# Performance work log

Measured on AMD Instinct MI355X. Metric: run time of the kernel, lower is better.

The kernel has to match this reference:

```python
import jax, jax.numpy as jnp
import numpy as np

D_HALF = 255
H = 2 * D_HALF + 1   # 511 channels (2*d+1)
L = 2048             # sequence length
N = 32               # S4D complex state modes per channel
NLAYERS = 4          # l
EPS = 1e-5


def setup_inputs() -> dict:
    key = jax.random.key(0)
    ks = jax.random.split(key, 10)
    Z = jax.random.normal(ks[0], (H, L), dtype=jnp.float32)
    # S4D-Lin initialization
    dt_min, dt_max = 1e-3, 1e-1
    log_dt = (jax.random.uniform(ks[1], (H,), dtype=jnp.float32)
              * (np.log(dt_max) - np.log(dt_min)) + np.log(dt_min))
    A_real_log = jnp.log(0.5 * jnp.ones((H, N), dtype=jnp.float32))
    A_imag = jnp.pi * jnp.broadcast_to(jnp.arange(N, dtype=jnp.float32), (H, N))
    C_re = jax.random.normal(ks[2], (H, N), dtype=jnp.float32)
    C_im = jax.random.normal(ks[3], (H, N), dtype=jnp.float32)
    D_skip = jax.random.normal(ks[4], (H,), dtype=jnp.float32)
    glu_w = jax.random.normal(ks[5], (2 * H, H), dtype=jnp.float32) / np.sqrt(H)
    glu_b = jnp.zeros((2 * H,), dtype=jnp.float32)
    ln_g = jnp.ones((H,), dtype=jnp.float32)
    ln_b = jnp.zeros((H,), dtype=jnp.float32)
    return {"Z": Z, "log_dt": log_dt, "A_real_log": A_real_log, "A_imag": A_imag,
            "C_re": C_re, "C_im": C_im, "D_skip": D_skip,
            "glu_w": glu_w, "glu_b": glu_b, "ln_g": ln_g, "ln_b": ln_b}


def _s4d_kernel(log_dt, A_real_log, A_imag, C_re, C_im):
    # A: (H,N) complex with negative real part; ZOH discretization kernel
    A = -jnp.exp(A_real_log) + 1j * A_imag
    dtA = A * jnp.exp(log_dt)[:, None]                  # (H,N)
    Ccoef = (C_re + 1j * C_im) * (jnp.exp(dtA) - 1.0) / A  # (H,N)
    V = jnp.exp(dtA[:, :, None] * jnp.arange(L, dtype=jnp.float32))  # (H,N,L)
    return 2.0 * jnp.einsum('hn,hnl->hl', Ccoef, V).real  # (H,L)


def _s4_block(Z, K, D_skip, glu_w, glu_b):
    # Z: (B,H,L); causal FFT convolution with kernel K (H,L)
    n = 2 * L
    Kf = jnp.fft.rfft(K, n=n)                  # (H, L+1)
    Uf = jnp.fft.rfft(Z, n=n)                  # (B,H,L+1)
    y = jnp.fft.irfft(Uf * Kf, n=n)[..., :L]   # (B,H,L)
    y = y + D_skip[:, None] * Z
    y = jax.nn.gelu(y)
    # output 1x1 conv H -> 2H followed by GLU over channels
    y2 = jnp.einsum('oh,bhl->bol', glu_w, y) + glu_b[:, None]
    return y2[:, :H] * jax.nn.sigmoid(y2[:, H:])


def _layernorm_channels(Z, g, b):
    # LayerNorm over the channel dim (module does norm(Z.transpose(-1,-2)).transpose(-1,-2))
    zt = jnp.swapaxes(Z, -1, -2)               # (B,L,H)
    mu = jnp.mean(zt, axis=-1, keepdims=True)
    var = jnp.mean((zt - mu) ** 2, axis=-1, keepdims=True)
    zt = (zt - mu) * jax.lax.rsqrt(var + EPS) * g + b
    return jnp.swapaxes(zt, -1, -2)


def reference(Z, log_dt, A_real_log, A_imag, C_re, C_im, D_skip, glu_w, glu_b, ln_g, ln_b):
    K = _s4d_kernel(log_dt, A_real_log, A_imag, C_re, C_im)
    z = Z[None]                                # unsqueeze(0) -> (1,H,L)
    for _ in range(NLAYERS):                   # mode='auto': shared layer, l iterations
        residual = z
        z = _s4_block(z, K, D_skip, glu_w, glu_b)
        z = z + residual
        z = _layernorm_channels(z, ln_g, ln_b)
    return z[0]                                # squeeze(0) -> (H,L)
```

## Files before the change

### kernel.cpp

```cpp
#include <hip/hip_runtime.h>
#include <hip/hip_bf16.h>
#include <math.h>

#define H 511
#define L 2048
#define NST 32
#define NLAYERS 4
#define LN_EPS 1e-5f
#define NCH 32
#define TC (L / NCH)
#define HN (H * NST)
#define HP 512
#define GBK 64
#define GBN 64
#define NSTRIPE 16

typedef __attribute__((ext_vector_type(8))) short short8;
typedef __attribute__((ext_vector_type(4))) float f32x4;

__device__ __forceinline__ ushort f2bf(float v) {
    __hip_bfloat16 b = __float2bfloat16(v);
    return *reinterpret_cast<ushort*>(&b);
}

__global__ __launch_bounds__(256) void pre_kernel(
    const float* __restrict__ log_dt,
    const float* __restrict__ A_real_log,
    const float* __restrict__ A_imag,
    const float* __restrict__ C_re,
    const float* __restrict__ C_im,
    const float* __restrict__ W,
    float* __restrict__ wr_o, float* __restrict__ wi_o,
    float* __restrict__ cr_o, float* __restrict__ ci_o,
    float* __restrict__ w64r_o, float* __restrict__ w64i_o,
    ushort* __restrict__ wbf)
{
    int idx = blockIdx.x * blockDim.x + threadIdx.x;
    if (idx < HN) {
        int h = idx / NST;
        float Ar = -expf(A_real_log[idx]);
        float Ai = A_imag[idx];
        float dt = expf(log_dt[h]);
        float dr = Ar * dt, di = Ai * dt;
        float er = expf(dr);
        float wr = er * cosf(di);
        float wi = er * sinf(di);
        float den = Ar * Ar + Ai * Ai;
        float a = wr - 1.0f, b = wi;
        float inv = 1.0f / den;
        float qr = (a * Ar + b * Ai) * inv;
        float qi = (b * Ar - a * Ai) * inv;
        wr_o[idx] = wr; wi_o[idx] = wi;
        cr_o[idx] = 2.0f * (C_re[idx] * qr - C_im[idx] * qi);
        ci_o[idx] = 2.0f * (C_re[idx] * qi + C_im[idx] * qr);
        float sr = wr, si = wi;
        #pragma unroll
        for (int k = 0; k < 6; ++k) {
            float nr = sr * sr - si * si;
            float ni = 2.0f * sr * si;
            sr = nr; si = ni;
        }
        w64r_o[idx] = sr; w64i_o[idx] = si;
    }
    if (idx < 2 * H * HP) {
        int r = idx / HP, k = idx % HP;
        float v = (k < H) ? W[(size_t)r * H + k] : 0.0f;
        wbf[idx] = f2bf(v);
    }
}

template <int CTRL, int ROW_MASK>
__device__ __forceinline__ float dpp_add(float x) {
    int r = __builtin_amdgcn_update_dpp(0, __float_as_int(x), CTRL, ROW_MASK, 0xf, true);
    return x + __int_as_float(r);
}
__device__ __forceinline__ float reduce32_to_lane31(float p) {
    p = dpp_add<0x111, 0xf>(p);
    p = dpp_add<0x112, 0xf>(p);
    p = dpp_add<0x114, 0xf>(p);
    p = dpp_add<0x118, 0xf>(p);
    p = dpp_add<0x142, 0xa>(p);
    return p;
}

__device__ __forceinline__ float gelu_tanh(float v) {
    const float c0 = 0.7978845608028654f;
    float t = tanhf(c0 * (v + 0.044715f * v * v * v));
    return 0.5f * v * (1.0f + t);
}

__global__ __launch_bounds__(1024, 8) void conv_fused(
    const float* __restrict__ z,
    const float* __restrict__ wr_,
    const float* __restrict__ wi_,
    const float* __restrict__ cr_,
    const float* __restrict__ ci_,
    const float* __restrict__ w64r_,
    const float* __restrict__ w64i_,
    const float* __restrict__ D_skip,
    ushort* __restrict__ yb)
{
    __shared__ float zs[L];
    __shared__ float ber[NCH][NST];
    __shared__ float bei[NCH][NST];
    __shared__ float ysf[L];

    const int tid  = threadIdx.x;
    const int wv   = tid >> 6;
    const int half = (tid >> 5) & 1;
    const int ln   = tid & 31;
    const int c    = wv * 2 + half;
    const int h    = blockIdx.x;

    *(float2*)&zs[tid * 2] = *(const float2*)&z[(size_t)h * L + tid * 2];

    const int cidx = h * NST + ln;
    const float wr = wr_[cidx], wi = wi_[cidx];
    const float cr = cr_[cidx], ci = ci_[cidx];
    const float Dh = D_skip[h];
    __syncthreads();

    float sr = 0.f, si = 0.f;
    {
        const float* zp = &zs[c * TC];
        #pragma unroll 8
        for (int l = 0; l < TC; ++l) {
            float zl = zp[l];
            float nsr = fmaf(wr, sr, fmaf(-wi, si, zl));
            float nsi = fmaf(wr, si, wi * sr);
            sr = nsr; si = nsi;
        }
    }
    ber[c][ln] = sr;
    bei[c][ln] = si;
    __syncthreads();

    {
        const int lam = tid & 63;
        const int c2 = lam & 31;
        const int n2 = ((tid >> 6) << 1) | (lam >> 5);
        float Ir = ber[c2][n2], Ii = bei[c2][n2];
        float Wr = w64r_[h * NST + n2], Wi = w64i_[h * NST + n2];
        #pragma unroll
        for (int d = 1; d < 32; d <<= 1) {
            float pr = __shfl_up(Ir, d, 32);
            float pi = __shfl_up(Ii, d, 32);
            if (c2 < d) { pr = 0.f; pi = 0.f; }
            float tr = fmaf(Wr, pr, -Wi * pi);
            float ti = fmaf(Wr, pi,  Wi * pr);
            Ir += tr; Ii += ti;
            float nWr = Wr * Wr - Wi * Wi;
            float nWi = 2.0f * Wr * Wi;
            Wr = nWr; Wi = nWi;
        }
        float Cr = __shfl_up(Ir, 1, 32);
        float Ci = __shfl_up(Ii, 1, 32);
        if (c2 == 0) { Cr = 0.f; Ci = 0.f; }
        __syncthreads();
        ber[c2][n2] = Cr;
        bei[c2][n2] = Ci;
    }
    __syncthreads();

    sr = ber[c][ln];
    si = bei[c][ln];
    {
        const float* zp = &zs[c * TC];
        float* yp = &ysf[c * TC];
        #pragma unroll 4
        for (int l = 0; l < TC; ++l) {
            float zl = zp[l];
            float nsr = fmaf(wr, sr, fmaf(-wi, si, zl));
            float nsi = fmaf(wr, si, wi * sr);
            sr = nsr; si = nsi;
            float p = fmaf(cr, sr, -ci * si);
            p = reduce32_to_lane31(p);
            if (ln == 31) yp[l] = fmaf(Dh, zl, p);
        }
    }
    __syncthreads();

    {
        ushort2 v;
        v.x = f2bf(gelu_tanh(ysf[tid * 2]));
        v.y = f2bf(gelu_tanh(ysf[tid * 2 + 1]));
        *(ushort2*)&yb[(size_t)h * L + tid * 2] = v;
    }
}

__global__ __launch_bounds__(256) void glu_mfma(
    const ushort* __restrict__ wbf,
    const ushort* __restrict__ yb,
    const float* __restrict__ bias,
    const float* __restrict__ zres,
    float* __restrict__ out,
    float* __restrict__ psum,
    float* __restrict__ psq)
{
    __shared__ ushort As1[32 * GBK];
    __shared__ ushort As2[32 * GBK];
    __shared__ ushort Bs[GBN * GBK];
    __shared__ ushort tempT[4][32 * 40];
    __shared__ float  sls[2][64];
    __shared__ float  slq[2][64];

    const int tid = threadIdx.x;
    const int h0 = blockIdx.y * 32;
    const int l0 = blockIdx.x * GBN;
    const int wid = tid >> 6;
    const int lane = tid & 63;
    const int wrow = (wid >> 1) * 16;
    const int wcol = (wid & 1) * 32;

    f32x4 acc1[2] = {{0.f,0.f,0.f,0.f},{0.f,0.f,0.f,0.f}};
    f32x4 acc2[2] = {{0.f,0.f,0.f,0.f},{0.f,0.f,0.f,0.f}};

    const int ar = tid >> 3;
    const int ak = tid & 7;
    const int hq1 = (h0 + ar < H) ? (h0 + ar) : (H - 1);
    const int hq2 = hq1 + H;
    const int aswz = ak ^ (ar & 7);

    const int tm   = tid >> 6;
    const int t64  = tid & 63;
    const int ksub = (tm & 1) * 32;
    const int lsub = (tm >> 1) * 32;
    const int bkl  = t64 >> 1;
    const int bhalf= t64 & 1;
    const int blr  = t64 >> 1;
    const int bkh  = t64 & 1;

    for (int k0 = 0; k0 < HP; k0 += GBK) {
        {
            short8 va1 = *(const short8*)&wbf[(size_t)hq1 * HP + k0 + ak * 8];
            short8 va2 = *(const short8*)&wbf[(size_t)hq2 * HP + k0 + ak * 8];
            *(short8*)&As1[ar * GBK + aswz * 8] = va1;
            *(short8*)&As2[ar * GBK + aswz * 8] = va2;
        }
        {
            const int kg = k0 + ksub + bkl;
            short8 v0 = {0,0,0,0,0,0,0,0}, v1 = {0,0,0,0,0,0,0,0};
            if (kg < H) {
                const ushort* row = &yb[(size_t)kg * L + l0 + lsub + bhalf * 16];
                v0 = *(const short8*)&row[0];
                v1 = *(const short8*)&row[8];
            }
            ushort* tp = &tempT[tm][0];
            #pragma unroll
            for (int j = 0; j < 8; ++j)
                tp[(bhalf * 16 + j) * 40 + bkl] = (ushort)v0[j];
            #pragma unroll
            for (int j = 0; j < 8; ++j)
                tp[(bhalf * 16 + 8 + j) * 40 + bkl] = (ushort)v1[j];
        }
        __syncthreads();
        {
            const ushort* tp = &tempT[tm][0];
            short8 b0 = *(const short8*)&tp[blr * 40 + bkh * 16];
            short8 b1 = *(const short8*)&tp[blr * 40 + bkh * 16 + 8];
            const int L_ = lsub + blr;
            const int kg0 = (ksub >> 3) + bkh * 2;
            *(short8*)&Bs[L_ * GBK + ((kg0    ) ^ (L_ & 7)) * 8] = b0;
            *(short8*)&Bs[L_ * GBK + ((kg0 + 1) ^ (L_ & 7)) * 8] = b1;
        }
        __syncthreads();

        #pragma unroll
        for (int kk = 0; kk < 2; ++kk) {
            const int arow = wrow + (lane & 15);
            const int kg = kk * 4 + (lane >> 4);
            short8 a1 = *(const short8*)&As1[arow * GBK + (kg ^ (arow & 7)) * 8];
            short8 a2 = *(const short8*)&As2[arow * GBK + (kg ^ (arow & 7)) * 8];
            #pragma unroll
            for (int nf = 0; nf < 2; ++nf) {
                const int brow = wcol + nf * 16 + (lane & 15);
                short8 b = *(const short8*)&Bs[brow * GBK + (kg ^ (brow & 7)) * 8];
                acc1[nf] = __builtin_amdgcn_mfma_f32_16x16x32_bf16(a1, b, acc1[nf], 0, 0, 0);
                acc2[nf] = __builtin_amdgcn_mfma_f32_16x16x32_bf16(a2, b, acc2[nf], 0, 0, 0);
            }
        }
        __syncthreads();
    }

    float ps[2] = {0.f, 0.f}, pq[2] = {0.f, 0.f};
    #pragma unroll
    for (int nf = 0; nf < 2; ++nf) {
        const int col = l0 + wcol + nf * 16 + (lane & 15);
        #pragma unroll
        for (int r = 0; r < 4; ++r) {
            const int h = h0 + wrow + (lane >> 4) * 4 + r;
            if (h < H) {
                float v1 = acc1[nf][r] + bias[h];
                float v2 = acc2[nf][r] + bias[h + H];
                float o = v1 * (1.0f / (1.0f + expf(-v2))) + zres[(size_t)h * L + col];
                out[(size_t)h * L + col] = o;
                ps[nf] += o;
                pq[nf] = fmaf(o, o, pq[nf]);
            }
        }
    }
    #pragma unroll
    for (int nf = 0; nf < 2; ++nf) {
        ps[nf] += __shfl_xor(ps[nf], 16, 64);
        ps[nf] += __shfl_xor(ps[nf], 32, 64);
        pq[nf] += __shfl_xor(pq[nf], 16, 64);
        pq[nf] += __shfl_xor(pq[nf], 32, 64);
        if ((lane >> 4) == 0) {
            int cl = wcol + nf * 16 + lane;
            sls[wid >> 1][cl] = ps[nf];
            slq[wid >> 1][cl] = pq[nf];
        }
    }
    __syncthreads();
    if (tid < 64) {
        psum[(size_t)blockIdx.y * L + l0 + tid] = sls[0][tid] + sls[1][tid];
        psq [(size_t)blockIdx.y * L + l0 + tid] = slq[0][tid] + slq[1][tid];
    }
}

__global__ __launch_bounds__(256) void ln_apply(
    const float* __restrict__ zpre,
    const float* __restrict__ psum, const float* __restrict__ psq,
    const float* __restrict__ g, const float* __restrict__ b,
    float* __restrict__ out)
{
    const int tx = threadIdx.x & 63;
    const int ty = threadIdx.x >> 6;
    const int l = blockIdx.x * 64 + tx;
    const int s = blockIdx.y;

    float S = 0.f, Q = 0.f;
    #pragma unroll
    for (int k = 0; k < NSTRIPE; ++k) {
        S += psum[(size_t)k * L + l];
        Q += psq[(size_t)k * L + l];
    }
    const float invH = 1.0f / (float)H;
    float mu = S * invH;
    float var = Q * invH - mu * mu;
    float rstd = rsqrtf(var + LN_EPS);

    const int hbase = s * 32;
    #pragma unroll
    for (int j = 0; j < 8; ++j) {
        int h = hbase + ty + j * 4;
        if (h < H) {
            float v = zpre[(size_t)h * L + l];
            out[(size_t)h * L + l] = (v - mu) * rstd * g[h] + b[h];
        }
    }
}

extern "C" void kernel_launch(void* const* d_in, const int* in_sizes, int n_in,
                              void* d_out, int out_size, void* d_ws, size_t ws_size,
                              hipStream_t stream) {
    const float* Z          = (const float*)d_in[0];
    const float* log_dt     = (const float*)d_in[1];
    const float* A_real_log = (const float*)d_in[2];
    const float* A_imag     = (const float*)d_in[3];
    const float* C_re       = (const float*)d_in[4];
    const float* C_im       = (const float*)d_in[5];
    const float* D_skip     = (const float*)d_in[6];
    const float* glu_w      = (const float*)d_in[7];
    const float* glu_b      = (const float*)d_in[8];
    const float* ln_g       = (const float*)d_in[9];
    const float* ln_b       = (const float*)d_in[10];

    float* out = (float*)d_out;
    float* ws  = (float*)d_ws;

    float* wr    = ws;
    float* wi    = wr + HN;
    float* cr    = wi + HN;
    float* ci    = cr + HN;
    float* w64r  = ci + HN;
    float* w64i  = w64r + HN;
    float* zbuf  = w64i + HN;
    float* psum  = zbuf + (size_t)H * L;
    float* psq   = psum + (size_t)NSTRIPE * L;
    ushort* yb  = (ushort*)(psq + (size_t)NSTRIPE * L);
    ushort* wbf = yb + (size_t)H * L;

    pre_kernel<<<(2 * H * HP + 255) / 256, 256, 0, stream>>>(
        log_dt, A_real_log, A_imag, C_re, C_im, glu_w,
        wr, wi, cr, ci, w64r, w64i, wbf);

    const dim3 gg(L / GBN, (H + 31) / 32);
    const dim3 lg(L / 64, NSTRIPE);

    for (int layer = 0; layer < NLAYERS; ++layer) {
        const float* zcur = (layer == 0) ? Z : zbuf;

        conv_fused<<<H, 1024, 0, stream>>>(
            zcur, wr, wi, cr, ci, w64r, w64i, D_skip, yb);
        glu_mfma<<<gg, 256, 0, stream>>>(wbf, yb, glu_b, zcur, out, psum, psq);

        float* lnout = (layer < NLAYERS - 1) ? zbuf : out;
        ln_apply<<<lg, 256, 0, stream>>>(out, psum, psq, ln_g, ln_b, lnout);
    }
}
```

Measured before the change: 232.2 us.

## Fuse layernorm apply into next layer's conv kernel load stage

The per-layer ln_apply launch is removed. The next conv_fused kernel now reduces the stripe partial sums and normalizes its input row while loading it, and writes the normalized row to zbuf so the GLU residual can use it. Only one final ln_apply runs, working in place on the output. Shared-memory rows for ber/bei are also padded by one element to avoid bank conflicts. Each conv block now redundantly reads the 16-stripe partial sums for all 2048 positions, which adds global traffic per channel block.

```diff
diff --git a/kernel.cpp b/kernel.cpp
--- a/kernel.cpp
+++ b/kernel.cpp
@@ -90,7 +90,12 @@
 }
 
 __global__ __launch_bounds__(1024, 8) void conv_fused(
-    const float* __restrict__ z,
+    const float* __restrict__ zsrc,
+    const float* __restrict__ psum_p,
+    const float* __restrict__ psq_p,
+    const float* __restrict__ lng,
+    const float* __restrict__ lnb,
+    const int donorm,
     const float* __restrict__ wr_,
     const float* __restrict__ wi_,
     const float* __restrict__ cr_,
@@ -98,11 +103,12 @@
     const float* __restrict__ w64r_,
     const float* __restrict__ w64i_,
     const float* __restrict__ D_skip,
+    float* __restrict__ znorm,
     ushort* __restrict__ yb)
 {
     __shared__ float zs[L];
-    __shared__ float ber[NCH][NST];
-    __shared__ float bei[NCH][NST];
+    __shared__ float ber[NCH][NST + 1];
+    __shared__ float bei[NCH][NST + 1];
     __shared__ float ysf[L];
 
     const int tid  = threadIdx.x;
@@ -112,7 +118,29 @@
     const int c    = wv * 2 + half;
     const int h    = blockIdx.x;
 
-    *(float2*)&zs[tid * 2] = *(const float2*)&z[(size_t)h * L + tid * 2];
+    {
+        const int c0 = tid * 2;
+        float2 v = *(const float2*)&zsrc[(size_t)h * L + c0];
+        if (donorm) {
+            float2 S = {0.f, 0.f}, Q = {0.f, 0.f};
+            #pragma unroll
+            for (int k = 0; k < NSTRIPE; ++k) {
+                float2 sv = *(const float2*)&psum_p[(size_t)k * L + c0];
+                float2 qv = *(const float2*)&psq_p[(size_t)k * L + c0];
+                S.x += sv.x; S.y += sv.y;
+                Q.x += qv.x; Q.y += qv.y;
+            }
+            const float invH = 1.0f / (float)H;
+            float mu0 = S.x * invH, mu1 = S.y * invH;
+            float rs0 = rsqrtf(Q.x * invH - mu0 * mu0 + LN_EPS);
+            float rs1 = rsqrtf(Q.y * invH - mu1 * mu1 + LN_EPS);
+            float gh = lng[h], bh = lnb[h];
+            v.x = (v.x - mu0) * rs0 * gh + bh;
+            v.y = (v.y - mu1) * rs1 * gh + bh;
+        }
+        *(float2*)&zs[c0] = v;
+        *(float2*)&znorm[(size_t)h * L + c0] = v;
+    }
 
     const int cidx = h * NST + ln;
     const float wr = wr_[cidx], wi = wi_[cidx];
@@ -319,7 +347,6 @@
 }
 
 __global__ __launch_bounds__(256) void ln_apply(
-    const float* __restrict__ zpre,
     const float* __restrict__ psum, const float* __restrict__ psq,
     const float* __restrict__ g, const float* __restrict__ b,
     float* __restrict__ out)
@@ -345,7 +372,7 @@
     for (int j = 0; j < 8; ++j) {
         int h = hbase + ty + j * 4;
         if (h < H) {
-            float v = zpre[(size_t)h * L + l];
+            float v = out[(size_t)h * L + l];
             out[(size_t)h * L + l] = (v - mu) * rstd * g[h] + b[h];
         }
     }
@@ -389,13 +416,14 @@
     const dim3 lg(L / 64, NSTRIPE);
 
     for (int layer = 0; layer < NLAYERS; ++layer) {
-        const float* zcur = (layer == 0) ? Z : zbuf;
+        const int donorm = (layer > 0);
+        const float* zsrc = (layer == 0) ? Z : out;
 
         conv_fused<<<H, 1024, 0, stream>>>(
-            zcur, wr, wi, cr, ci, w64r, w64i, D_skip, yb);
-        glu_mfma<<<gg, 256, 0, stream>>>(wbf, yb, glu_b, zcur, out, psum, psq);
-
-        float* lnout = (layer < NLAYERS - 1) ? zbuf : out;
-        ln_apply<<<lg, 256, 0, stream>>>(out, psum, psq, ln_g, ln_b, lnout);
-    }
-}
+            zsrc, psum, psq, ln_g, ln_b, donorm,
+            wr, wi, cr, ci, w64r, w64i, D_skip, zbuf, yb);
+
+        glu_mfma<<<gg, 256, 0, stream>>>(wbf, yb, glu_b, zbuf, out, psum, psq);
+    }
+    ln_apply<<<lg, 256, 0, stream>>>(psum, psq, ln_g, ln_b, out);
+}
```

New measurement: 239.7 us. +3.2%, slower.
